# Performance work log

Measured on AMD Instinct MI355X. Metric: run time of the kernel, lower is better.

## Reference

```python
import jax, jax.numpy as jnp
import numpy as np

B, S, D = 4, 2048, 1024
H = 16
HD = D // H

def setup_inputs() -> dict:
    key = jax.random.key(0)
    ks = jax.random.split(key, 6)
    std = 1.0 / np.sqrt(D)
    x = jax.random.normal(ks[0], (B, S, D), dtype=jnp.float32)
    Wq = jax.random.uniform(ks[1], (D, D), jnp.float32, -std, std)
    Wk = jax.random.uniform(ks[2], (D, D), jnp.float32, -std, std)
    Wv = jax.random.uniform(ks[3], (D, D), jnp.float32, -std, std)
    Wo = jax.random.uniform(ks[4], (D, D), jnp.float32, -std, std)
    bo = jax.random.uniform(ks[5], (D,), jnp.float32, -std, std)
    return {"x": x, "Wq": Wq, "Wk": Wk, "Wv": Wv, "Wo": Wo, "bo": bo}

def reference(x, Wq, Wk, Wv, Wo, bo):
    b, s, _ = x.shape
    # projections; torch Linear computes x @ W^T, here W stored as (d_in, d_out)... we use (D, D) applied as x @ W
    q = (x @ Wq).reshape(b, s, H, HD).transpose(0, 2, 1, 3)  # b h s hd
    k = (x @ Wk).reshape(b, s, H, HD).transpose(0, 2, 1, 3)
    v = (x @ Wv).reshape(b, s, H, HD).transpose(0, 2, 1, 3)
    scores = jnp.einsum('bhqd,bhkd->bhqk', q, k)
    causal = jnp.triu(jnp.ones((s, s), dtype=bool), k=1)
    scores = jnp.where(causal[None, None], -jnp.inf, scores)
    attn = jax.nn.softmax(scores / np.sqrt(HD), axis=-1)  # dropout=0.0 -> identity
    ctx = jnp.einsum('bhqk,bhkd->bhqd', attn, v)
    ctx = ctx.transpose(0, 2, 1, 3).reshape(b, s, D)
    return ctx @ Wo + bo
```

## Files before the change

### kernel.cpp

```cpp
#include <hip/hip_runtime.h>

typedef unsigned short u16;
typedef __bf16 bf16x8 __attribute__((ext_vector_type(8)));
typedef float f32x4 __attribute__((ext_vector_type(4)));

#define Bn 4
#define Sn 2048
#define Dn 1024
#define Hn 16
#define HDn 64

__device__ inline u16 f2bf(float f) {
  unsigned u = __builtin_bit_cast(unsigned, f);
  u += 0x7fffu + ((u >> 16) & 1u);
  return (u16)(u >> 16);
}

__device__ __forceinline__ void gl2lds16(const u16* g, u16* l) {
  __builtin_amdgcn_global_load_lds(
      (const __attribute__((address_space(1))) unsigned int*)g,
      (__attribute__((address_space(3))) unsigned int*)l, 16, 0, 0);
}

__device__ __forceinline__ float fexp2(float x) {
  return __builtin_amdgcn_exp2f(x);
}

__device__ __forceinline__ unsigned pk_bf_trunc(float lo, float hi) {
  return __builtin_amdgcn_perm(__builtin_bit_cast(unsigned, hi),
                               __builtin_bit_cast(unsigned, lo), 0x07060302u);
}

__global__ __launch_bounds__(256) void cvt4(const float* __restrict__ in,
                                            u16* __restrict__ out, int n4) {
  int i = blockIdx.x * 256 + threadIdx.x;
  if (i < n4) {
    float4 v = ((const float4*)in)[i];
    ushort4 o;
    o.x = f2bf(v.x); o.y = f2bf(v.y); o.z = f2bf(v.z); o.w = f2bf(v.w);
    ((ushort4*)out)[i] = o;
  }
}

__global__ __launch_bounds__(256) void tcvt4(const float* __restrict__ w0,
                                             const float* __restrict__ w1,
                                             const float* __restrict__ w2,
                                             const float* __restrict__ w3,
                                             u16* __restrict__ out) {
  __shared__ u16 tile[32][33];
  const float* in = (blockIdx.z == 0) ? w0 : (blockIdx.z == 1) ? w1
                   : (blockIdx.z == 2) ? w2 : w3;
  u16* dst = out + (size_t)blockIdx.z * Dn * Dn;
  int bx = blockIdx.x * 32;
  int by = blockIdx.y * 32;
  int tx = threadIdx.x & 31;
  int ty = threadIdx.x >> 5;
#pragma unroll
  for (int r = 0; r < 32; r += 8)
    tile[ty + r][tx] = f2bf(in[(size_t)(by + ty + r) * Dn + bx + tx]);
  __syncthreads();
#pragma unroll
  for (int r = 0; r < 32; r += 8)
    dst[(size_t)(bx + ty + r) * Dn + by + tx] = tile[tx][ty + r];
}

__global__ __launch_bounds__(512, 2) void gemm_qkv(const u16* __restrict__ A,
                                                   const u16* __restrict__ Bt,
                                                   u16* __restrict__ qkb,
                                                   u16* __restrict__ vt,
                                                   float qscale) {
  __shared__ __attribute__((aligned(16))) u16 S[2][4][8192];

  const int tid = threadIdx.x;
  const int lane = tid & 63;
  const int lcol = lane & 15;
  const int quad = lane >> 4;
  const int wave = tid >> 6;
  const int wr = wave >> 2;
  const int wc = wave & 3;

  const int bid = blockIdx.x;
  const int bm = ((bid & 7) * 4 + ((bid >> 3) & 3)) * 256;
  const int bn = (bid >> 5) * 256;

  const u16* srcp[4][2];
#pragma unroll
  for (int rg = 0; rg < 4; rg++) {
#pragma unroll
    for (int j = 0; j < 2; j++) {
      int o = j * 8192 + tid * 16;
      int l = o ^ (((o >> 8) & 7) << 4);
      int rho = l >> 7;
      int c2 = (l >> 1) & 63;
      int gr;
      if (rg == 0)      gr = bm + (rho & 63) + ((rho >> 6) << 7);
      else if (rg == 1) gr = bm + 64 + (rho & 63) + ((rho >> 6) << 7);
      else if (rg == 2) gr = bn + ((rho >> 5) << 6) + (rho & 31);
      else              gr = bn + ((rho >> 5) << 6) + 32 + (rho & 31);
      const u16* base = (rg < 2) ? A : Bt;
      srcp[rg][j] = base + (size_t)gr * Dn + c2;
    }
  }

  auto stg = [&](int rg, int buf, int tile) {
    if (tile >= 16) return;
    const int k0 = tile << 6;
    u16* d = &S[buf][rg][tid * 8];
    gl2lds16(srcp[rg][0] + k0, d);
    gl2lds16(srcp[rg][1] + k0, d + 4096);
  };

  f32x4 acc[8][4];
#pragma unroll
  for (int i = 0; i < 8; i++)
#pragma unroll
    for (int j = 0; j < 4; j++) acc[i][j] = (f32x4){0.f, 0.f, 0.f, 0.f};

  const int SW = (lcol & 14) << 3;
  const int cs0 = (quad * 16) ^ SW;
  const int cs1 = (64 + quad * 16) ^ SW;

  bf16x8 bk0[4], bk1[4];

#define MFMA16(a, b, c) __builtin_amdgcn_mfma_f32_16x16x32_bf16(a, b, c, 0, 0, 0)

#define ARD(D, Q, F, K)                                                      \
  (*(const bf16x8*)((const char*)&S[D][(Q) >> 1][0] +                        \
      ((wr * 64 + ((Q) & 1) * 32 + (F) * 16 + lcol) * 128 +                  \
       ((K) ? cs1 : cs0))))
#define BRD(D, NI, K)                                                        \
  (*(const bf16x8*)((const char*)&S[D][2 + ((NI) >> 1)][0] +                 \
      ((wc * 32 + ((NI) & 1) * 16 + lcol) * 128 + ((K) ? cs1 : cs0))))

#define PHASE(D, T, Q, DO_B, STG_RG, WAIT)                                   \
  {                                                                          \
    bf16x8 a00 = ARD(D, Q, 0, 0), a01 = ARD(D, Q, 0, 1);                     \
    bf16x8 a10 = ARD(D, Q, 1, 0), a11 = ARD(D, Q, 1, 1);                     \
    if (DO_B) {                                                              \
      _Pragma("unroll") for (int ni = 0; ni < 4; ni++) {                     \
        bk0[ni] = BRD(D, ni, 0);                                             \
        bk1[ni] = BRD(D, ni, 1);                                             \
      }                                                                      \
    }                                                                        \
    stg(STG_RG, (D) ^ 1, (T) + 1);                                           \
    WAIT;                                                                    \
    __builtin_amdgcn_s_barrier();                                            \
    asm volatile("s_waitcnt lgkmcnt(0)" ::: "memory");                       \
    __builtin_amdgcn_sched_barrier(0);                                       \
    __builtin_amdgcn_s_setprio(1);                                           \
    _Pragma("unroll") for (int ni = 0; ni < 4; ni++) {                       \
      acc[(Q) * 2][ni] = MFMA16(a00, bk0[ni], acc[(Q) * 2][ni]);             \
      acc[(Q) * 2][ni] = MFMA16(a01, bk1[ni], acc[(Q) * 2][ni]);             \
      acc[(Q) * 2 + 1][ni] = MFMA16(a10, bk0[ni], acc[(Q) * 2 + 1][ni]);     \
      acc[(Q) * 2 + 1][ni] = MFMA16(a11, bk1[ni], acc[(Q) * 2 + 1][ni]);     \
    }                                                                        \
    __builtin_amdgcn_s_setprio(0);                                           \
    __builtin_amdgcn_s_barrier();                                            \
  }

#define TILE(D, T)                                                           \
  PHASE(D, T, 0, 1, 2, )                                                     \
  PHASE(D, T, 1, 0, 3,                                                       \
        if ((T) < 15) asm volatile("s_waitcnt vmcnt(4)" ::: "memory");       \
        else asm volatile("s_waitcnt vmcnt(0)" ::: "memory"))                \
  PHASE(D, T, 2, 0, 0, )                                                     \
  PHASE(D, T, 3, 0, 1, asm volatile("s_waitcnt vmcnt(2)" ::: "memory"))

  stg(2, 0, 0); stg(3, 0, 0); stg(0, 0, 0); stg(1, 0, 0);
  asm volatile("s_waitcnt vmcnt(2)" ::: "memory");
  __builtin_amdgcn_s_barrier();

#pragma unroll 1
  for (int I = 0; I < 8; ++I) {
    const int T0 = 2 * I, T1 = 2 * I + 1;
    TILE(0, T0)
    TILE(1, T1)
  }
#undef TILE
#undef PHASE
#undef ARD
#undef BRD
#undef MFMA16

  const int rb = bm + wr * 128 + quad * 4;
  const int cb = bn + wc * 64 + lcol;
  if (bn >= 2048) {
#pragma unroll
    for (int ai = 0; ai < 8; ai++) {
#pragma unroll
      for (int bj = 0; bj < 4; bj++) {
        int row0 = rb + ((ai >> 2) << 6) + ((ai & 3) << 4);
        int s = row0 & (Sn - 1);
        int bb = row0 >> 11;
        int vcol = cb + ((bj >> 1) << 5) + ((bj & 1) << 4) - 2048;
        int bh = (bb << 4) + (vcol >> 6);
        int hd = vcol & 63;
        unsigned d0 = (unsigned)f2bf(acc[ai][bj][0]) |
                      ((unsigned)f2bf(acc[ai][bj][1]) << 16);
        unsigned d1 = (unsigned)f2bf(acc[ai][bj][2]) |
                      ((unsigned)f2bf(acc[ai][bj][3]) << 16);
        *(uint2*)(vt + ((size_t)bh * HDn + hd) * Sn + s) = (uint2){d0, d1};
      }
    }
  } else {
    const float scale = (bn < 1024) ? qscale : 1.0f;
#pragma unroll
    for (int ai = 0; ai < 8; ai++) {
#pragma unroll
      for (int bj = 0; bj < 4; bj++) {
        int row0 = rb + ((ai >> 2) << 6) + ((ai & 3) << 4);
        int col = cb + ((bj >> 1) << 5) + ((bj & 1) << 4);
#pragma unroll
        for (int r = 0; r < 4; r++)
          qkb[(size_t)(row0 + r) * 2048 + col] = f2bf(acc[ai][bj][r] * scale);
      }
    }
  }
}

__global__ __launch_bounds__(256) void gemm_out(const u16* __restrict__ A,
                                                const u16* __restrict__ Bt,
                                                float* __restrict__ Cout,
                                                const float* __restrict__ bias) {
  __shared__ __attribute__((aligned(16))) u16 As[2][2][128][32];
  __shared__ __attribute__((aligned(16))) u16 Bs[2][2][128][32];
  const int K = Dn;
  const int t = threadIdx.x;
  const int wave = t >> 6;
  const int lane = t & 63;
  const int lcol = lane & 15;
  const int quad = lane >> 4;
  const int wm = (wave >> 1) * 64;
  const int wn = (wave & 1) * 64;
  const int bm = blockIdx.y * 128;
  const int bn = blockIdx.x * 128;

  const int srow = lane >> 2;
  const int sseg = (lane & 3) * 8;
  const u16* a0p = A + (size_t)(bm + wave * 16 + srow) * K + sseg;
  const u16* a1p = a0p + (size_t)64 * K;
  const u16* b0p = Bt + (size_t)(bn + wave * 16 + srow) * K + sseg;
  const u16* b1p = b0p + (size_t)64 * K;
  u16* asl = &As[0][0][0][0] + wave * 512 + lane * 8;
  u16* bsl = &Bs[0][0][0][0] + wave * 512 + lane * 8;

  auto stage = [&](int k0, int d) {
    u16* as = asl + d * 8192;
    u16* bs = bsl + d * 8192;
    gl2lds16(a0p + k0, as);
    gl2lds16(a1p + k0, as + 2048);
    gl2lds16(a0p + k0 + 32, as + 4096);
    gl2lds16(a1p + k0 + 32, as + 6144);
    gl2lds16(b0p + k0, bs);
    gl2lds16(b1p + k0, bs + 2048);
    gl2lds16(b0p + k0 + 32, bs + 4096);
    gl2lds16(b1p + k0 + 32, bs + 6144);
  };

  f32x4 acc[4][4];
#pragma unroll
  for (int i = 0; i < 4; i++)
#pragma unroll
    for (int j = 0; j < 4; j++) acc[i][j] = (f32x4){0.f, 0.f, 0.f, 0.f};

  stage(0, 0);
  int d = 0;
  for (int k0 = 0; k0 < K; k0 += 64, d ^= 1) {
    __syncthreads();
    if (k0 + 64 < K) stage(k0 + 64, d ^ 1);
#pragma unroll
    for (int ks = 0; ks < 2; ks++) {
      bf16x8 af[4], bf[4];
#pragma unroll
      for (int mi = 0; mi < 4; mi++)
        af[mi] = *(const bf16x8*)(&As[d][ks][wm + mi * 16 + lcol][quad * 8]);
#pragma unroll
      for (int ni = 0; ni < 4; ni++)
        bf[ni] = *(const bf16x8*)(&Bs[d][ks][wn + ni * 16 + lcol][quad * 8]);
#pragma unroll
      for (int mi = 0; mi < 4; mi++)
#pragma unroll
        for (int ni = 0; ni < 4; ni++)
          acc[mi][ni] = __builtin_amdgcn_mfma_f32_16x16x32_bf16(af[mi], bf[ni], acc[mi][ni], 0, 0, 0);
    }
  }

#pragma unroll
  for (int mi = 0; mi < 4; mi++) {
#pragma unroll
    for (int ni = 0; ni < 4; ni++) {
#pragma unroll
      for (int r = 0; r < 4; r++) {
        int row = bm + wm + mi * 16 + quad * 4 + r;
        int col = bn + wn + ni * 16 + lcol;
        Cout[(size_t)row * Dn + col] = acc[mi][ni][r] + bias[col];
      }
    }
  }
}

__global__ __launch_bounds__(256, 2) void attn5(const u16* __restrict__ QK,
                                                const u16* __restrict__ Vt,
                                                u16* __restrict__ ctx) {
  __shared__ __attribute__((aligned(16))) u16 Ks2[2][64][32];
  __shared__ __attribute__((aligned(16))) u16 Vts2[2][64][32];
  __shared__ __attribute__((aligned(16))) u16 Pt[4][32][72];

  const int bh = blockIdx.x;
  const int b = bh >> 4, h = bh & 15;
  const int pair = blockIdx.y;
  const int t = threadIdx.x;
  const int w = t >> 6;
  const int lane = t & 63;
  const int lcol = lane & 15;
  const int quad = lane >> 4;
  const int qw0 = pair * 128 + w * 32;
  const int qw1 = (15 - pair) * 128 + w * 32;

  const size_t qkbase = ((size_t)b * Sn) * 2048 + h * HDn;
  const size_t obase = ((size_t)b * Sn) * Dn + h * HDn;
  const size_t vbase = ((size_t)bh * HDn) * Sn;

  bf16x8 qf[2][2][2];
#pragma unroll
  for (int si = 0; si < 2; si++) {
    const int qws = si ? qw1 : qw0;
#pragma unroll
    for (int qb = 0; qb < 2; qb++) {
      const u16* qp = QK + qkbase + (size_t)(qws + qb * 16 + lcol) * 2048 + quad * 8;
      qf[si][qb][0] = *(const bf16x8*)qp;
      qf[si][qb][1] = *(const bf16x8*)(qp + 32);
    }
  }

  f32x4 o[2][2][4];
#pragma unroll
  for (int si = 0; si < 2; si++)
#pragma unroll
    for (int qb = 0; qb < 2; qb++)
#pragma unroll
      for (int nb = 0; nb < 4; nb++) o[si][qb][nb] = (f32x4){0.f, 0.f, 0.f, 0.f};
  float lsum[2][2] = {{0.f, 0.f}, {0.f, 0.f}};

  const int srow = lane >> 2;
  const int sseg = (lane & 3) * 8;
  const u16* kp0 = QK + qkbase + 1024 + (size_t)(w * 16 + srow) * 2048 + sseg;
  const u16* vp0 = Vt + vbase + (size_t)(w * 16 + srow) * Sn + sseg;
  u16* ksl0 = &Ks2[0][0][0] + w * 512 + lane * 8;
  u16* ksl1 = ksl0 + 2048;
  u16* vsl0 = &Vts2[0][0][0] + w * 512 + lane * 8;
  u16* vsl1 = vsl0 + 2048;

  auto do_strip = [&](int si, int qw, int j0) {
    f32x4 s[4][2];
#pragma unroll
    for (int mb = 0; mb < 4; mb++) {
      bf16x8 kf0 = *(const bf16x8*)(&Ks2[0][mb * 16 + lcol][quad * 8]);
      bf16x8 kf1 = *(const bf16x8*)(&Ks2[1][mb * 16 + lcol][quad * 8]);
#pragma unroll
      for (int qb = 0; qb < 2; qb++) {
        f32x4 a = (f32x4){0.f, 0.f, 0.f, 0.f};
        a = __builtin_amdgcn_mfma_f32_16x16x32_bf16(kf0, qf[si][qb][0], a, 0, 0, 0);
        a = __builtin_amdgcn_mfma_f32_16x16x32_bf16(kf1, qf[si][qb][1], a, 0, 0, 0);
        s[mb][qb] = a;
      }
    }

    const bool needmask = (j0 + 63 > qw);
#pragma unroll
    for (int qb = 0; qb < 2; qb++) {
      const int qrow = qw + qb * 16 + lcol;
#pragma unroll
      for (int mb = 0; mb < 4; mb++) {
        float p[4];
#pragma unroll
        for (int r = 0; r < 4; r++) p[r] = fexp2(s[mb][qb][r]);
        if (needmask) {
          const int kvb = j0 + mb * 16 + quad * 4;
#pragma unroll
          for (int r = 0; r < 4; r++)
            if (kvb + r > qrow) p[r] = 0.f;
        }
        lsum[si][qb] += (p[0] + p[1]) + (p[2] + p[3]);
        unsigned d0 = pk_bf_trunc(p[0], p[1]);
        unsigned d1 = pk_bf_trunc(p[2], p[3]);
        *(uint2*)(&Pt[w][qb * 16 + lcol][mb * 16 + quad * 4]) = (uint2){d0, d1};
      }
    }

#pragma unroll
    for (int c = 0; c < 2; c++) {
      bf16x8 pf0 = *(const bf16x8*)(&Pt[w][lcol][c * 32 + quad * 8]);
      bf16x8 pf1 = *(const bf16x8*)(&Pt[w][16 + lcol][c * 32 + quad * 8]);
#pragma unroll
      for (int nb = 0; nb < 4; nb++) {
        bf16x8 vf = *(const bf16x8*)(&Vts2[c][nb * 16 + lcol][quad * 8]);
        o[si][0][nb] = __builtin_amdgcn_mfma_f32_16x16x32_bf16(vf, pf0, o[si][0][nb], 0, 0, 0);
        o[si][1][nb] = __builtin_amdgcn_mfma_f32_16x16x32_bf16(vf, pf1, o[si][1][nb], 0, 0, 0);
      }
    }
  };

  const int n_kv = (15 - pair) * 128 + 128;

  for (int j0 = 0; j0 < n_kv; j0 += 64) {
    {
      const u16* kp = kp0 + (size_t)j0 * 2048;
      gl2lds16(kp, ksl0);
      gl2lds16(kp + 32, ksl1);
      const u16* vp = vp0 + j0;
      gl2lds16(vp, vsl0);
      gl2lds16(vp + 32, vsl1);
    }
    __syncthreads();

    if (j0 <= qw1 + 31) do_strip(1, qw1, j0);
    if (j0 <= qw0 + 31) do_strip(0, qw0, j0);
    __syncthreads();
  }

#pragma unroll
  for (int si = 0; si < 2; si++) {
    const int qws = si ? qw1 : qw0;
#pragma unroll
    for (int qb = 0; qb < 2; qb++) {
      float l = lsum[si][qb];
      l += __shfl_xor(l, 16);
      l += __shfl_xor(l, 32);
      float inv = 1.0f / l;
#pragma unroll
      for (int nb = 0; nb < 4; nb++) {
        unsigned d0 = (unsigned)f2bf(o[si][qb][nb][0] * inv) |
                      ((unsigned)f2bf(o[si][qb][nb][1] * inv) << 16);
        unsigned d1 = (unsigned)f2bf(o[si][qb][nb][2] * inv) |
                      ((unsigned)f2bf(o[si][qb][nb][3] * inv) << 16);
        u16* p = ctx + obase + (size_t)(qws + qb * 16 + lcol) * Dn + nb * 16 + quad * 4;
        *(uint2*)p = (uint2){d0, d1};
      }
    }
  }
}

extern "C" void kernel_launch(void* const* d_in, const int* in_sizes, int n_in,
                              void* d_out, int out_size, void* d_ws, size_t ws_size,
                              hipStream_t stream) {
  const float* x  = (const float*)d_in[0];
  const float* Wq = (const float*)d_in[1];
  const float* Wk = (const float*)d_in[2];
  const float* Wv = (const float*)d_in[3];
  const float* Wo = (const float*)d_in[4];
  const float* bo = (const float*)d_in[5];
  float* out = (float*)d_out;

  const size_t BSD = (size_t)Bn * Sn * Dn;
  const size_t DD = (size_t)Dn * Dn;

  u16* xb    = (u16*)d_ws;
  u16* wall  = xb + BSD;
  u16* qkb   = wall + 4 * DD;
  u16* vt    = qkb + 2 * BSD;
  u16* cb    = vt + BSD;

  cvt4<<<(int)(BSD / 4 / 256), 256, 0, stream>>>(x, xb, (int)(BSD / 4));
  tcvt4<<<dim3(Dn / 32, Dn / 32, 4), 256, 0, stream>>>(Wq, Wk, Wv, Wo, wall);

  gemm_qkv<<<dim3(384), 512, 0, stream>>>(xb, wall, qkb, vt,
                                          0.125f * 1.44269504f);

  attn5<<<dim3(Bn * Hn, 8), 256, 0, stream>>>(qkb, vt, cb);

  gemm_out<<<dim3(Dn / 128, (Bn * Sn) / 128), 256, 0, stream>>>(cb, wall + 3 * DD, out, bo);
}
```

Before: 241.4 us.

## Shrink QKV GEMM tile to 128x256 with triple-buffered LDS pipeline

The QKV projection GEMM now uses 128x256 block tiles instead of 256x256, doubling the grid to 768 blocks, and cuts the accumulator array in half. The LDS staging moves from double buffering to a three-deep ring, prefetching two K-tiles ahead with adjusted vmcnt waits. The aim is better CU occupancy and load balance across the larger grid, and more latency hiding from the deeper prefetch. The cost is less operand reuse per block, so more global traffic per FLOP.

Result: slower. 247.5 us (+2.5%).

```diff
diff --git a/kernel.cpp b/kernel.cpp
--- a/kernel.cpp
+++ b/kernel.cpp
@@ -69,7 +69,7 @@
                                                    u16* __restrict__ qkb,
                                                    u16* __restrict__ vt,
                                                    float qscale) {
-  __shared__ __attribute__((aligned(16))) u16 S[2][4][8192];
+  __shared__ __attribute__((aligned(16))) u16 S[3][3][8192];
 
   const int tid = threadIdx.x;
   const int lane = tid & 63;
@@ -80,12 +80,13 @@
   const int wc = wave & 3;
 
   const int bid = blockIdx.x;
-  const int bm = ((bid & 7) * 4 + ((bid >> 3) & 3)) * 256;
-  const int bn = (bid >> 5) * 256;
-
-  const u16* srcp[4][2];
-#pragma unroll
-  for (int rg = 0; rg < 4; rg++) {
+  const int idx = bid >> 3;
+  const int bm = (((bid & 7) << 3) + (idx & 7)) * 128;
+  const int bn = (idx >> 3) * 256;
+
+  const u16* srcp[3][2];
+#pragma unroll
+  for (int rg = 0; rg < 3; rg++) {
 #pragma unroll
     for (int j = 0; j < 2; j++) {
       int o = j * 8192 + tid * 16;
@@ -93,11 +94,10 @@
       int rho = l >> 7;
       int c2 = (l >> 1) & 63;
       int gr;
-      if (rg == 0)      gr = bm + (rho & 63) + ((rho >> 6) << 7);
-      else if (rg == 1) gr = bm + 64 + (rho & 63) + ((rho >> 6) << 7);
-      else if (rg == 2) gr = bn + ((rho >> 5) << 6) + (rho & 31);
+      if (rg == 0)      gr = bm + rho;
+      else if (rg == 1) gr = bn + ((rho >> 5) << 6) + (rho & 31);
       else              gr = bn + ((rho >> 5) << 6) + 32 + (rho & 31);
-      const u16* base = (rg < 2) ? A : Bt;
+      const u16* base = (rg == 0) ? A : Bt;
       srcp[rg][j] = base + (size_t)gr * Dn + c2;
     }
   }
@@ -110,9 +110,9 @@
     gl2lds16(srcp[rg][1] + k0, d + 4096);
   };
 
-  f32x4 acc[8][4];
-#pragma unroll
-  for (int i = 0; i < 8; i++)
+  f32x4 acc[4][4];
+#pragma unroll
+  for (int i = 0; i < 4; i++)
 #pragma unroll
     for (int j = 0; j < 4; j++) acc[i][j] = (f32x4){0.f, 0.f, 0.f, 0.f};
 
@@ -125,14 +125,13 @@
 #define MFMA16(a, b, c) __builtin_amdgcn_mfma_f32_16x16x32_bf16(a, b, c, 0, 0, 0)
 
 #define ARD(D, Q, F, K)                                                      \
-  (*(const bf16x8*)((const char*)&S[D][(Q) >> 1][0] +                        \
-      ((wr * 64 + ((Q) & 1) * 32 + (F) * 16 + lcol) * 128 +                  \
-       ((K) ? cs1 : cs0))))
+  (*(const bf16x8*)((const char*)&S[D][0][0] +                               \
+      ((wr * 64 + (Q) * 32 + (F) * 16 + lcol) * 128 + ((K) ? cs1 : cs0))))
 #define BRD(D, NI, K)                                                        \
-  (*(const bf16x8*)((const char*)&S[D][2 + ((NI) >> 1)][0] +                 \
+  (*(const bf16x8*)((const char*)&S[D][1 + ((NI) >> 1)][0] +                 \
       ((wc * 32 + ((NI) & 1) * 16 + lcol) * 128 + ((K) ? cs1 : cs0))))
 
-#define PHASE(D, T, Q, DO_B, STG_RG, WAIT)                                   \
+#define PHASE(D, Q, DO_B, STG_STMT, WAIT_STMT)                               \
   {                                                                          \
     bf16x8 a00 = ARD(D, Q, 0, 0), a01 = ARD(D, Q, 0, 1);                     \
     bf16x8 a10 = ARD(D, Q, 1, 0), a11 = ARD(D, Q, 1, 1);                     \
@@ -142,8 +141,8 @@
         bk1[ni] = BRD(D, ni, 1);                                             \
       }                                                                      \
     }                                                                        \
-    stg(STG_RG, (D) ^ 1, (T) + 1);                                           \
-    WAIT;                                                                    \
+    STG_STMT;                                                                \
+    WAIT_STMT;                                                               \
     __builtin_amdgcn_s_barrier();                                            \
     asm volatile("s_waitcnt lgkmcnt(0)" ::: "memory");                       \
     __builtin_amdgcn_sched_barrier(0);                                       \
@@ -158,61 +157,62 @@
     __builtin_amdgcn_s_barrier();                                            \
   }
 
-#define TILE(D, T)                                                           \
-  PHASE(D, T, 0, 1, 2, )                                                     \
-  PHASE(D, T, 1, 0, 3,                                                       \
-        if ((T) < 15) asm volatile("s_waitcnt vmcnt(4)" ::: "memory");       \
-        else asm volatile("s_waitcnt vmcnt(0)" ::: "memory"))                \
-  PHASE(D, T, 2, 0, 0, )                                                     \
-  PHASE(D, T, 3, 0, 1, asm volatile("s_waitcnt vmcnt(2)" ::: "memory"))
-
-  stg(2, 0, 0); stg(3, 0, 0); stg(0, 0, 0); stg(1, 0, 0);
-  asm volatile("s_waitcnt vmcnt(2)" ::: "memory");
+#define TILE(D, DN, T)                                                       \
+  PHASE(D, 0, 1, { stg(1, DN, (T) + 2); stg(0, DN, (T) + 2); }, )            \
+  PHASE(D, 1, 0, { stg(2, DN, (T) + 2); },                                   \
+        if ((T) < 14) asm volatile("s_waitcnt vmcnt(6)" ::: "memory");       \
+        else if ((T) == 14) asm volatile("s_waitcnt vmcnt(0)" ::: "memory"))
+
+  stg(1, 0, 0); stg(0, 0, 0); stg(2, 0, 0);
+  stg(1, 1, 1); stg(0, 1, 1); stg(2, 1, 1);
+  asm volatile("s_waitcnt vmcnt(6)" ::: "memory");
   __builtin_amdgcn_s_barrier();
 
 #pragma unroll 1
-  for (int I = 0; I < 8; ++I) {
-    const int T0 = 2 * I, T1 = 2 * I + 1;
-    TILE(0, T0)
-    TILE(1, T1)
-  }
+  for (int I = 0; I < 5; ++I) {
+    const int T0 = 3 * I;
+    TILE(0, 2, T0)
+    TILE(1, 0, T0 + 1)
+    TILE(2, 1, T0 + 2)
+  }
+  TILE(0, 2, 15)
 #undef TILE
 #undef PHASE
 #undef ARD
 #undef BRD
 #undef MFMA16
 
-  const int rb = bm + wr * 128 + quad * 4;
+  const int rb = bm + wr * 64 + quad * 4;
   const int cb = bn + wc * 64 + lcol;
   if (bn >= 2048) {
 #pragma unroll
-    for (int ai = 0; ai < 8; ai++) {
-#pragma unroll
-      for (int bj = 0; bj < 4; bj++) {
-        int row0 = rb + ((ai >> 2) << 6) + ((ai & 3) << 4);
+    for (int mi = 0; mi < 4; mi++) {
+#pragma unroll
+      for (int ni = 0; ni < 4; ni++) {
+        int row0 = rb + mi * 16;
         int s = row0 & (Sn - 1);
         int bb = row0 >> 11;
-        int vcol = cb + ((bj >> 1) << 5) + ((bj & 1) << 4) - 2048;
+        int vcol = cb + ni * 16 - 2048;
         int bh = (bb << 4) + (vcol >> 6);
         int hd = vcol & 63;
-        unsigned d0 = (unsigned)f2bf(acc[ai][bj][0]) |
-                      ((unsigned)f2bf(acc[ai][bj][1]) << 16);
-        unsigned d1 = (unsigned)f2bf(acc[ai][bj][2]) |
-                      ((unsigned)f2bf(acc[ai][bj][3]) << 16);
+        unsigned d0 = (unsigned)f2bf(acc[mi][ni][0]) |
+                      ((unsigned)f2bf(acc[mi][ni][1]) << 16);
+        unsigned d1 = (unsigned)f2bf(acc[mi][ni][2]) |
+                      ((unsigned)f2bf(acc[mi][ni][3]) << 16);
         *(uint2*)(vt + ((size_t)bh * HDn + hd) * Sn + s) = (uint2){d0, d1};
       }
     }
   } else {
     const float scale = (bn < 1024) ? qscale : 1.0f;
 #pragma unroll
-    for (int ai = 0; ai < 8; ai++) {
-#pragma unroll
-      for (int bj = 0; bj < 4; bj++) {
-        int row0 = rb + ((ai >> 2) << 6) + ((ai & 3) << 4);
-        int col = cb + ((bj >> 1) << 5) + ((bj & 1) << 4);
+    for (int mi = 0; mi < 4; mi++) {
+#pragma unroll
+      for (int ni = 0; ni < 4; ni++) {
+        int row0 = rb + mi * 16;
+        int col = cb + ni * 16;
 #pragma unroll
         for (int r = 0; r < 4; r++)
-          qkb[(size_t)(row0 + r) * 2048 + col] = f2bf(acc[ai][bj][r] * scale);
+          qkb[(size_t)(row0 + r) * 2048 + col] = f2bf(acc[mi][ni][r] * scale);
       }
     }
   }
@@ -464,7 +464,7 @@
   cvt4<<<(int)(BSD / 4 / 256), 256, 0, stream>>>(x, xb, (int)(BSD / 4));
   tcvt4<<<dim3(Dn / 32, Dn / 32, 4), 256, 0, stream>>>(Wq, Wk, Wv, Wo, wall);
 
-  gemm_qkv<<<dim3(384), 512, 0, stream>>>(xb, wall, qkb, vt,
+  gemm_qkv<<<dim3(768), 512, 0, stream>>>(xb, wall, qkb, vt,
                                           0.125f * 1.44269504f);
 
   attn5<<<dim3(Bn * Hn, 8), 256, 0, stream>>>(qkb, vt, cb);
```
